# Kernel optimization log

Hardware: AMD Instinct MI355X
Metric: run time of the kernel (lower is better)

Reference implementation:

```python
import jax, jax.numpy as jnp
import numpy as np

HEADS = 8
DH = 64          # value head dim == kernel head dim (expansion ratio 1.0)
DIM = 256
BOT = 256        # bottleneck_dim
DOUT = 256
HID = 4 * 256    # MLP hidden (expansion_ratio=4)
EPS_LN = 1e-5
EPS_GN = 1e-6


def layer_norm(x, g, b):
    m = x.mean(axis=-1, keepdims=True)
    v = x.var(axis=-1, keepdims=True)
    return (x - m) / jnp.sqrt(v + EPS_LN) * g + b


def rotate_half(x):
    x1, x2 = jnp.split(x, 2, axis=-1)
    return jnp.concatenate([-x2, x1], axis=-1)


def apply_rope(t, cos, sin):
    return t * cos + rotate_half(t) * sin


def mlp(x, W1, b1, W2, b2):
    return jax.nn.gelu(x @ W1 + b1) @ W2 + b2


def pooling_reducer(x, Win, W1, b1, W2, b2):
    # x: (b, n, m, c); mean-pool over axis 2, then MLP
    x = x @ Win
    x = x.mean(axis=2)
    return mlp(x, W1, b1, W2, b2)


def dp_kernel(x, Wqk, cos, sin):
    # x: (b, n, BOT) -> softmax attention kernel (b, h, n, n)
    b, n, _ = x.shape
    qk = (x @ Wqk).reshape(b, n, 2, HEADS, DH).transpose(0, 3, 2, 1, 4)  # b h 2 n d
    qk = apply_rope(qk, cos, sin)
    q, k = qk[:, :, 0], qk[:, :, 1]
    attn = jnp.einsum('bhid,bhjd->bhij', q, k) * (1.0 / DH)  # softmax scale = 1/dim_head
    return jax.nn.softmax(attn, axis=-1)


def group_norm(x):
    # channels-last GroupNorm(heads groups, affine=False), per position
    b, i, l, _ = x.shape
    xg = x.reshape(b, i, l, HEADS, DH)
    m = xg.mean(axis=-1, keepdims=True)
    v = xg.var(axis=-1, keepdims=True)
    return ((xg - m) / jnp.sqrt(v + EPS_GN)).reshape(b, i, l, HEADS * DH)


def setup_inputs() -> dict:
    key = jax.random.key(0)
    ks = jax.random.split(key, 32)
    B, NY, NX = 4, 128, 128
    s = 0.02
    d = {
        'u': jax.random.normal(ks[0], (B, NY, NX, DIM), jnp.float32),
        'rotary_cos_y': jax.random.uniform(ks[1], (NY, DH), jnp.float32),
        'rotary_sin_y': jax.random.uniform(ks[2], (NY, DH), jnp.float32),
        'rotary_cos_x': jax.random.uniform(ks[3], (NX, DH), jnp.float32),
        'rotary_sin_x': jax.random.uniform(ks[4], (NX, DH), jnp.float32),
        'scalar_cond': jax.random.normal(ks[5], (B,), jnp.float32),
        # norms
        'ln1_g': jnp.ones((DIM,), jnp.float32), 'ln1_b': jnp.zeros((DIM,), jnp.float32),
        'ln2_g': jnp.ones((DIM,), jnp.float32), 'ln2_b': jnp.zeros((DIM,), jnp.float32),
        # to_v
        'Wv': jax.random.normal(ks[6], (DIM, HEADS * DH), jnp.float32) * s,
        # to_y PoolingReducer
        'Wy_in': jax.random.normal(ks[7], (DIM, DIM), jnp.float32) * s,
        'Wy1': jax.random.normal(ks[8], (DIM, HID), jnp.float32) * s,
        'by1': jnp.zeros((HID,), jnp.float32),
        'Wy2': jax.random.normal(ks[9], (HID, BOT), jnp.float32) * s,
        'by2': jnp.zeros((BOT,), jnp.float32),
        # to_x PoolingReducer
        'Wx_in': jax.random.normal(ks[10], (DIM, DIM), jnp.float32) * s,
        'Wx1': jax.random.normal(ks[11], (DIM, HID), jnp.float32) * s,
        'bx1': jnp.zeros((HID,), jnp.float32),
        'Wx2': jax.random.normal(ks[12], (HID, BOT), jnp.float32) * s,
        'bx2': jnp.zeros((BOT,), jnp.float32),
        # kernels
        'Wqk_x': jax.random.normal(ks[13], (BOT, 2 * HEADS * DH), jnp.float32) * s,
        'Wqk_y': jax.random.normal(ks[14], (BOT, 2 * HEADS * DH), jnp.float32) * s,
        # merge head
        'Wm': jax.random.normal(ks[15], (HEADS * DH, DOUT), jnp.float32) * s,
        'bm': jnp.zeros((DOUT,), jnp.float32),
        # ffn
        'Wf1': jax.random.normal(ks[16], (DOUT, 4 * DOUT), jnp.float32) * s,
        'bf1': jnp.zeros((4 * DOUT,), jnp.float32),
        'Wf2': jax.random.normal(ks[17], (4 * DOUT, DOUT), jnp.float32) * s,
        'bf2': jnp.zeros((DOUT,), jnp.float32),
    }
    return d


def reference(u, rotary_cos_y, rotary_sin_y, rotary_cos_x, rotary_sin_x, scalar_cond,
              ln1_g, ln1_b, ln2_g, ln2_b, Wv,
              Wy_in, Wy1, by1, Wy2, by2,
              Wx_in, Wx1, bx1, Wx2, bx2,
              Wqk_x, Wqk_y, Wm, bm, Wf1, bf1, Wf2, bf2):
    b, ny, nx, _ = u.shape
    u_skip = u
    un = layer_norm(u, ln1_g, ln1_b)
    # to_x: transpose grid then pool over (now) second spatial axis -> (b, nx, BOT)
    u_x = pooling_reducer(un.transpose(0, 2, 1, 3), Wx_in, Wx1, bx1, Wx2, bx2)
    # to_y: pool over nx -> (b, ny, BOT)
    u_y = pooling_reducer(un, Wy_in, Wy1, by1, Wy2, by2)
    k_x = dp_kernel(u_x, Wqk_x, rotary_cos_x, rotary_sin_x)  # (b,h,nx,nx)
    k_y = dp_kernel(u_y, Wqk_y, rotary_cos_y, rotary_sin_y)  # (b,h,ny,ny)
    # values: b i l (h c) -> b h i l c
    v = (un @ Wv).reshape(b, ny, nx, HEADS, DH).transpose(0, 3, 1, 2, 4)
    u_phi = jnp.einsum('bhij,bhjmc->bhimc', k_y, v)
    u_phi = jnp.einsum('bhlm,bhimc->bhilc', k_x, u_phi)
    u_phi = u_phi.transpose(0, 2, 3, 1, 4).reshape(b, ny, nx, HEADS * DH)
    u2 = group_norm(u_phi) @ Wm + bm + u_skip  # dropout is identity in eval
    out = mlp(layer_norm(u2, ln2_g, ln2_b), Wf1, bf1, Wf2, bf2) + u2
    return out
```

## Files before the change

### kernel.cpp

```cpp
#include <hip/hip_runtime.h>
#include <hip/hip_bf16.h>
#include <math.h>

#define NB 4
#define NY 128
#define NX 128
#define DIM 256
#define NH 8
#define DH_ 64
#define HDIM 512
#define HID 1024
#define NPOS (NB*NY*NX)

typedef __hip_bfloat16 bf16_t;
typedef __attribute__((ext_vector_type(8))) short short8;
typedef __attribute__((ext_vector_type(4))) float f32x4;

__device__ __forceinline__ float b2f(bf16_t x){ return __bfloat162float(x); }
__device__ __forceinline__ bf16_t f2b(float x){ return __float2bfloat16(x); }
__device__ __forceinline__ short f2s(float x){ bf16_t h = __float2bfloat16(x); return *reinterpret_cast<short*>(&h); }
__device__ __forceinline__ float s2f(short x){ bf16_t h = *reinterpret_cast<bf16_t*>(&x); return __bfloat162float(h); }


__device__ __forceinline__ float gelu_tanh(float x){
  float z = 1.5957691216057308f*(x + 0.044715f*x*x*x);
  return x / (1.0f + __expf(-z));
}

__global__ void __launch_bounds__(256) k_pack(const float* __restrict__ W,
    short* __restrict__ out, int K, int N){
  int tid = blockIdx.x*256 + threadIdx.x;
  int lane = tid & 63;
  int rem = tid >> 6;
  int ntiles = N >> 4;
  int nt = rem % ntiles, kb = rem / ntiles;
  int n = nt*16 + (lane & 15);
  int k0 = kb*32 + (lane>>4)*8;
  short8 v;
  #pragma unroll
  for (int j=0;j<8;j++) v[j] = f2s(W[(size_t)(k0+j)*N + n]);
  *(short8*)&out[(size_t)tid*8] = v;
}

__global__ void __launch_bounds__(256) k_ln1(const float* __restrict__ u,
    const float* __restrict__ g, const float* __restrict__ b,
    bf16_t* __restrict__ un){
  int wave = threadIdx.x >> 6, lane = threadIdx.x & 63;
  size_t row = (size_t)blockIdx.x*4 + wave;
  const float* x = u + row*DIM;
  float v[4]; float s=0.f, ss=0.f;
  #pragma unroll
  for (int j=0;j<4;j++){ float t = x[lane + j*64]; v[j]=t; s+=t; ss+=t*t; }
  #pragma unroll
  for (int off=32;off>0;off>>=1){ s += __shfl_down(s,off,64); ss += __shfl_down(ss,off,64); }
  s = __shfl(s,0,64); ss = __shfl(ss,0,64);
  float m = s*(1.0f/DIM);
  float var = ss*(1.0f/DIM) - m*m;
  float r = rsqrtf(var + 1e-5f);
  bf16_t* o = un + row*DIM;
  #pragma unroll
  for (int j=0;j<4;j++){
    int f = lane + j*64;
    o[f] = f2b((v[j]-m)*r*g[f] + b[f]);
  }
}

__global__ void __launch_bounds__(256) k_pool_y(const bf16_t* __restrict__ un, float* __restrict__ pooly){
  int by = blockIdx.x;
  int d = threadIdx.x;
  size_t base = (size_t)by*NX*DIM + d;
  float s = 0.f;
  for (int x=0;x<NX;x++) s += b2f(un[base + (size_t)x*DIM]);
  pooly[(size_t)by*DIM + d] = s*(1.0f/NX);
}
__global__ void __launch_bounds__(256) k_pool_x(const bf16_t* __restrict__ un, float* __restrict__ poolx){
  int bb = blockIdx.x / NX, x = blockIdx.x % NX;
  int d = threadIdx.x;
  size_t base = ((size_t)bb*NY*NX + x)*DIM + d;
  float s = 0.f;
  for (int y=0;y<NY;y++) s += b2f(un[base + (size_t)y*NX*DIM]);
  poolx[(size_t)blockIdx.x*DIM + d] = s*(1.0f/NY);
}

#define GS_STRIDE 72
__global__ void __launch_bounds__(256) k_gemm2(const float* __restrict__ A0,
    const float* __restrict__ A1,
    const short* __restrict__ W0, const short* __restrict__ W1,
    const float* __restrict__ b0, const float* __restrict__ b1,
    float* __restrict__ C0, float* __restrict__ C1, int N, int K, int dogelu){
  const float* A  = blockIdx.z ? A1 : A0;
  const short* WP = blockIdx.z ? W1 : W0;
  const float* bias = blockIdx.z ? b1 : b0;
  float* C = blockIdx.z ? C1 : C0;
  __shared__ __align__(16) short As[64*GS_STRIDE];
  int tid = threadIdx.x;
  int lane = tid & 63, w = tid >> 6;
  int am = lane & 15, aq = lane >> 4;
  int m0 = blockIdx.x*64;
  int nt0 = blockIdx.y*16;
  int ntiles = N >> 4;
  f32x4 o[4][4];
  #pragma unroll
  for (int mt=0;mt<4;mt++)
    #pragma unroll
    for (int nt=0;nt<4;nt++) o[mt][nt] = (f32x4){0.f,0.f,0.f,0.f};

  for (int kc=0; kc<K; kc+=64){
    #pragma unroll
    for (int it=0; it<4; it++){
      int q = tid + it*256;
      int r = q >> 4, c4 = q & 15;
      float4 v = *(const float4*)&A[(size_t)(m0+r)*K + kc + c4*4];
      ushort4 p;
      p.x = (ushort)f2s(v.x); p.y = (ushort)f2s(v.y);
      p.z = (ushort)f2s(v.z); p.w = (ushort)f2s(v.w);
      *(ushort4*)&As[r*GS_STRIDE + c4*4] = p;
    }
    __syncthreads();
    #pragma unroll
    for (int kb=0; kb<2; kb++){
      short8 a[4], bfr[4];
      #pragma unroll
      for (int mt=0;mt<4;mt++)
        a[mt] = *(const short8*)&As[(mt*16+am)*GS_STRIDE + kb*32 + aq*8];
      int kbg = (kc>>5) + kb;
      #pragma unroll
      for (int nt=0;nt<4;nt++){
        int ntg = nt0 + w*4 + nt;
        bfr[nt] = *(const short8*)&WP[(size_t)((kbg*ntiles + ntg)*64 + lane)*8];
      }
      #pragma unroll
      for (int mt=0;mt<4;mt++)
        #pragma unroll
        for (int nt=0;nt<4;nt++)
          o[mt][nt] = __builtin_amdgcn_mfma_f32_16x16x32_bf16(a[mt], bfr[nt], o[mt][nt], 0,0,0);
    }
    __syncthreads();
  }

  #pragma unroll
  for (int nt=0;nt<4;nt++){
    int col = (nt0 + w*4 + nt)*16 + am;
    float bv = bias ? bias[col] : 0.f;
    #pragma unroll
    for (int mt=0;mt<4;mt++){
      #pragma unroll
      for (int reg=0;reg<4;reg++){
        int row = m0 + mt*16 + aq*4 + reg;
        float val = o[mt][nt][reg] + bv;
        if (dogelu) val = gelu_tanh(val);
        C[(size_t)row*N + col] = val;
      }
    }
  }
}

__global__ void __launch_bounds__(256) k_rope(const float* __restrict__ qk,
    const float* __restrict__ cs, const float* __restrict__ sn,
    float* __restrict__ q, float* __restrict__ k){
  int idx = blockIdx.x*256 + threadIdx.x;
  int c = idx & 63;
  int h = (idx>>6) & 7;
  int p = (idx>>9) & 1;
  int n = (idx>>10) & 127;
  int bb = idx>>17;
  float t = qk[idx];
  float t2 = qk[(c<32) ? idx+32 : idx-32];
  if (c<32) t2 = -t2;
  float val = t*cs[n*64+c] + t2*sn[n*64+c];
  float* dst = p ? k : q;
  dst[(((size_t)bb*NH + h)*128 + n)*64 + c] = val;
}

__global__ void __launch_bounds__(128) k_attn(const float* __restrict__ q,
    const float* __restrict__ k, bf16_t* __restrict__ attn){
  int i = blockIdx.x & 127;
  int bh = blockIdx.x >> 7;
  __shared__ float qs[64];
  __shared__ float sm[128];
  int tid = threadIdx.x;
  const float* qrow = q + ((size_t)bh*128 + i)*64;
  if (tid < 64) qs[tid] = qrow[tid];
  __syncthreads();
  const float* krow = k + ((size_t)bh*128 + tid)*64;
  float dot = 0.f;
  for (int c=0;c<64;c++) dot += qs[c]*krow[c];
  dot *= (1.0f/64.0f);
  sm[tid] = dot;
  __syncthreads();
  float mx = -1e30f;
  for (int j=0;j<128;j++) mx = fmaxf(mx, sm[j]);
  __syncthreads();
  float e = expf(dot - mx);
  sm[tid] = e;
  __syncthreads();
  float s = 0.f;
  for (int j=0;j<128;j++) s += sm[j];
  attn[(size_t)blockIdx.x*128 + tid] = f2b(e/s);
}

#define AST 136
#define UST 72
#define VST 136
__global__ void __launch_bounds__(256) k_phi1m(const bf16_t* __restrict__ un,
    const short* __restrict__ WvP, const bf16_t* __restrict__ attn,
    bf16_t* __restrict__ phi){
  int m  = blockIdx.x & (NX-1);
  int bh = blockIdx.x >> 7;
  int b  = bh >> 3, h = bh & 7;
  __shared__ __align__(16) short At[128*AST];
  __shared__ __align__(16) short unc[128*UST];
  __shared__ __align__(16) short Vt[64*VST];
  int tid = threadIdx.x;
  int lane = tid & 63, w = tid >> 6;
  int am = lane & 15, aq = lane >> 4;

  {
    const ushort* ag = (const ushort*)attn + (size_t)bh*16384;
    #pragma unroll
    for (int it=0; it<16; it++){
      int q = tid + it*256;
      int i = q >> 5, j4 = q & 31;
      *(ushort4*)&At[i*AST + j4*4] = *(const ushort4*)(ag + i*128 + j4*4);
    }
  }

  f32x4 v[2][4];
  #pragma unroll
  for (int mt=0;mt<2;mt++)
    #pragma unroll
    for (int nt=0;nt<4;nt++) v[mt][nt] = (f32x4){0.f,0.f,0.f,0.f};
  const ushort* ug = (const ushort*)un;
  for (int kc=0; kc<4; kc++){
    #pragma unroll
    for (int it=0; it<8; it++){
      int q = tid + it*256;
      int y = q >> 4, c4 = q & 15;
      *(ushort4*)&unc[y*UST + c4*4] =
          *(const ushort4*)(ug + (((size_t)b*NY + y)*NX + m)*DIM + kc*64 + c4*4);
    }
    __syncthreads();
    #pragma unroll
    for (int kb=0; kb<2; kb++){
      short8 a2[2], bb[4];
      #pragma unroll
      for (int mt=0;mt<2;mt++)
        a2[mt] = *(const short8*)&unc[(w*32 + mt*16 + am)*UST + kb*32 + aq*8];
      int kbg = kc*2 + kb;
      #pragma unroll
      for (int nt=0;nt<4;nt++)
        bb[nt] = *(const short8*)&WvP[(size_t)((kbg*32 + (h*4+nt))*64 + lane)*8];
      #pragma unroll
      for (int mt=0;mt<2;mt++)
        #pragma unroll
        for (int nt=0;nt<4;nt++)
          v[mt][nt] = __builtin_amdgcn_mfma_f32_16x16x32_bf16(a2[mt], bb[nt], v[mt][nt], 0,0,0);
    }
    __syncthreads();
  }
  #pragma unroll
  for (int mt=0;mt<2;mt++)
    #pragma unroll
    for (int nt=0;nt<4;nt++){
      int c = nt*16 + am;
      int y0 = w*32 + mt*16 + aq*4;
      ushort4 pk;
      pk.x = (ushort)f2s(v[mt][nt][0]);
      pk.y = (ushort)f2s(v[mt][nt][1]);
      pk.z = (ushort)f2s(v[mt][nt][2]);
      pk.w = (ushort)f2s(v[mt][nt][3]);
      *(ushort4*)&Vt[c*VST + y0] = pk;
    }
  __syncthreads();

  f32x4 o[2][4];
  #pragma unroll
  for (int mt=0;mt<2;mt++)
    #pragma unroll
    for (int nt=0;nt<4;nt++) o[mt][nt] = (f32x4){0.f,0.f,0.f,0.f};
  #pragma unroll
  for (int kb=0; kb<4; kb++){
    short8 a2[2], bb[4];
    #pragma unroll
    for (int mt=0;mt<2;mt++)
      a2[mt] = *(const short8*)&At[(w*32 + mt*16 + am)*AST + kb*32 + aq*8];
    #pragma unroll
    for (int nt=0;nt<4;nt++)
      bb[nt] = *(const short8*)&Vt[(nt*16 + am)*VST + kb*32 + aq*8];
    #pragma unroll
    for (int mt=0;mt<2;mt++)
      #pragma unroll
      for (int nt=0;nt<4;nt++)
        o[mt][nt] = __builtin_amdgcn_mfma_f32_16x16x32_bf16(a2[mt], bb[nt], o[mt][nt], 0,0,0);
  }
  ushort* pg = (ushort*)phi + (size_t)bh*NY*NX*DH_ + (size_t)m*DH_;
  #pragma unroll
  for (int mt=0;mt<2;mt++)
    #pragma unroll
    for (int nt=0;nt<4;nt++)
      #pragma unroll
      for (int reg=0;reg<4;reg++){
        int i = w*32 + mt*16 + aq*4 + reg;
        int c = nt*16 + am;
        pg[(size_t)i*(NX*DH_) + c] = (ushort)f2s(o[mt][nt][reg]);
      }
}

__global__ void __launch_bounds__(256) k_phi2m(const bf16_t* __restrict__ attn,
    bf16_t* __restrict__ phi){
  int i  = blockIdx.x & (NY-1);
  int bh = blockIdx.x >> 7;
  __shared__ __align__(16) short Ax[128*AST];
  __shared__ __align__(16) short Pt[64*VST];
  int tid = threadIdx.x;
  int lane = tid & 63, w = tid >> 6;
  int am = lane & 15, aq = lane >> 4;

  {
    const ushort* ag = (const ushort*)attn + (size_t)bh*16384;
    #pragma unroll
    for (int it=0; it<16; it++){
      int q = tid + it*256;
      int r = q >> 5, j4 = q & 31;
      *(ushort4*)&Ax[r*AST + j4*4] = *(const ushort4*)(ag + r*128 + j4*4);
    }
  }
  ushort* pg = (ushort*)phi + (size_t)(bh*NY + i)*(NX*DH_);
  #pragma unroll
  for (int it=0; it<8; it++){
    int q = tid + it*256;
    int mm = q >> 4, c4 = q & 15;
    ushort4 v4 = *(const ushort4*)(pg + mm*DH_ + c4*4);
    Pt[(c4*4+0)*VST + mm] = v4.x;
    Pt[(c4*4+1)*VST + mm] = v4.y;
    Pt[(c4*4+2)*VST + mm] = v4.z;
    Pt[(c4*4+3)*VST + mm] = v4.w;
  }
  __syncthreads();

  f32x4 o[2][4];
  #pragma unroll
  for (int mt=0;mt<2;mt++)
    #pragma unroll
    for (int nt=0;nt<4;nt++) o[mt][nt] = (f32x4){0.f,0.f,0.f,0.f};
  #pragma unroll
  for (int kb=0; kb<4; kb++){
    short8 a2[2], bb[4];
    #pragma unroll
    for (int mt=0;mt<2;mt++)
      a2[mt] = *(const short8*)&Ax[(w*32 + mt*16 + am)*AST + kb*32 + aq*8];
    #pragma unroll
    for (int nt=0;nt<4;nt++)
      bb[nt] = *(const short8*)&Pt[(nt*16 + am)*VST + kb*32 + aq*8];
    #pragma unroll
    for (int mt=0;mt<2;mt++)
      #pragma unroll
      for (int nt=0;nt<4;nt++)
        o[mt][nt] = __builtin_amdgcn_mfma_f32_16x16x32_bf16(a2[mt], bb[nt], o[mt][nt], 0,0,0);
  }
  #pragma unroll
  for (int mt=0;mt<2;mt++)
    #pragma unroll
    for (int nt=0;nt<4;nt++)
      #pragma unroll
      for (int reg=0;reg<4;reg++){
        int l = w*32 + mt*16 + aq*4 + reg;
        int c = nt*16 + am;
        pg[(size_t)l*DH_ + c] = (ushort)f2s(o[mt][nt][reg]);
      }
}

#define GN_ST 520
#define ML_ST 264
__global__ void __launch_bounds__(512, 4) k_tail(const bf16_t* __restrict__ phi,
    const short* __restrict__ WmP, const float* __restrict__ bm,
    const float* __restrict__ u,
    const float* __restrict__ g2, const float* __restrict__ b2,
    const short* __restrict__ Wf1P, const float* __restrict__ bf1,
    const short* __restrict__ Wf2P, const float* __restrict__ bf2,
    float* __restrict__ out){
  __shared__ __align__(16) short SMEM[64*ML_ST*2];
  __shared__ float mean_s[512], rstd_s[512];
  __shared__ float prow[64][4], prow2[64][4];
  __shared__ float mrow[64], rrow[64];
  short* Xg = SMEM;
  short* Xm = SMEM;
  short* H  = SMEM + 64*ML_ST;
  int tid = threadIdx.x;
  int lane = tid & 63, w = tid >> 6;
  int wh = w >> 2, wl = w & 3;
  int am = lane & 15, aq = lane >> 4;
  size_t p0 = (size_t)blockIdx.x*64;
  int b  = (int)(p0 >> 14);
  int y  = (int)((p0 >> 7) & 127);
  int x0 = (int)(p0 & 127);

  #pragma unroll
  for (int it=0; it<16; it++){
    int q = tid + it*512;
    int r = q >> 7, f4 = q & 127;
    int h = f4 >> 4, c4 = f4 & 15;
    const ushort* src = (const ushort*)phi +
        ((((size_t)b*NH + h)*NY + y)*NX + (x0 + r))*DH_ + c4*4;
    *(ushort4*)&Xg[r*GN_ST + f4*4] = *(const ushort4*)src;
  }
  __syncthreads();
  {
    int g = tid;
    int r = g >> 3, h = g & 7;
    const short* base = &Xg[r*GN_ST + h*64];
    float s=0.f, ss=0.f;
    #pragma unroll
    for (int i=0;i<16;i++){
      ushort4 v4 = *(const ushort4*)&base[i*4];
      float a = s2f((short)v4.x), bq = s2f((short)v4.y), cq = s2f((short)v4.z), d = s2f((short)v4.w);
      s += a+bq+cq+d; ss += a*a+bq*bq+cq*cq+d*d;
    }
    float mm = s*(1.0f/64.0f);
    float vv = ss*(1.0f/64.0f) - mm*mm;
    mean_s[g] = mm;
    rstd_s[g] = rsqrtf(vv + 1e-6f);
  }
  __syncthreads();
  #pragma unroll
  for (int it=0; it<16; it++){
    int q = tid + it*512;
    int r = q >> 7, f4 = q & 127;
    int h = f4 >> 4;
    float mm = mean_s[r*8 + h], rs = rstd_s[r*8 + h];
    short* ptr = &Xg[r*GN_ST + f4*4];
    ushort4 v4 = *(ushort4*)ptr;
    v4.x = (ushort)f2s((s2f((short)v4.x)-mm)*rs);
    v4.y = (ushort)f2s((s2f((short)v4.y)-mm)*rs);
    v4.z = (ushort)f2s((s2f((short)v4.z)-mm)*rs);
    v4.w = (ushort)f2s((s2f((short)v4.w)-mm)*rs);
    *(ushort4*)ptr = v4;
  }
  __syncthreads();

  f32x4 u2r[2][4];
  #pragma unroll
  for (int mt=0;mt<2;mt++)
    #pragma unroll
    for (int nt=0;nt<4;nt++) u2r[mt][nt] = (f32x4){0.f,0.f,0.f,0.f};
  for (int kb=0; kb<16; kb++){
    short8 a[2], bfr[4];
    #pragma unroll
    for (int mt=0;mt<2;mt++)
      a[mt] = *(const short8*)&Xg[(wh*32 + mt*16 + am)*GN_ST + kb*32 + aq*8];
    #pragma unroll
    for (int nt=0;nt<4;nt++)
      bfr[nt] = *(const short8*)&WmP[(size_t)((kb*16 + (wl*4+nt))*64 + lane)*8];
    #pragma unroll
    for (int mt=0;mt<2;mt++)
      #pragma unroll
      for (int nt=0;nt<4;nt++)
        u2r[mt][nt] = __builtin_amdgcn_mfma_f32_16x16x32_bf16(a[mt], bfr[nt], u2r[mt][nt], 0,0,0);
  }
  #pragma unroll
  for (int nt=0;nt<4;nt++){
    int col = wl*64 + nt*16 + am;
    float bmv = bm[col];
    #pragma unroll
    for (int mt=0;mt<2;mt++){
      #pragma unroll
      for (int reg=0;reg<4;reg++){
        size_t p = p0 + wh*32 + mt*16 + aq*4 + reg;
        u2r[mt][nt][reg] += bmv + u[p*DIM + col];
      }
    }
  }

  #pragma unroll
  for (int mt=0;mt<2;mt++){
    #pragma unroll
    for (int reg=0;reg<4;reg++){
      float s  = u2r[mt][0][reg]+u2r[mt][1][reg]+u2r[mt][2][reg]+u2r[mt][3][reg];
      float ss = u2r[mt][0][reg]*u2r[mt][0][reg]+u2r[mt][1][reg]*u2r[mt][1][reg]
               + u2r[mt][2][reg]*u2r[mt][2][reg]+u2r[mt][3][reg]*u2r[mt][3][reg];
      #pragma unroll
      for (int msk=1; msk<16; msk<<=1){
        s  += __shfl_xor(s,  msk, 64);
        ss += __shfl_xor(ss, msk, 64);
      }
      if (am == 0){
        int r = wh*32 + mt*16 + aq*4 + reg;
        prow[r][wl] = s;
        prow2[r][wl] = ss;
      }
    }
  }
  __syncthreads();
  if (tid < 64){
    float s  = prow[tid][0]+prow[tid][1]+prow[tid][2]+prow[tid][3];
    float ss = prow2[tid][0]+prow2[tid][1]+prow2[tid][2]+prow2[tid][3];
    float m = s*(1.0f/DIM);
    mrow[tid] = m;
    rrow[tid] = rsqrtf(ss*(1.0f/DIM) - m*m + 1e-5f);
  }
  __syncthreads();
  #pragma unroll
  for (int nt=0;nt<4;nt++){
    int col = wl*64 + nt*16 + am;
    float gg = g2[col], bb2 = b2[col];
    #pragma unroll
    for (int mt=0;mt<2;mt++){
      #pragma unroll
      for (int reg=0;reg<4;reg++){
        int r = wh*32 + mt*16 + aq*4 + reg;
        Xm[r*ML_ST + col] = f2s((u2r[mt][nt][reg]-mrow[r])*rrow[r]*gg + bb2);
      }
    }
  }
  __syncthreads();

  f32x4 o2[2][4];
  #pragma unroll
  for (int mt=0;mt<2;mt++)
    #pragma unroll
    for (int nt=0;nt<4;nt++) o2[mt][nt] = u2r[mt][nt];

  for (int nc=0; nc<4; nc++){
    f32x4 hacc[2][4];
    #pragma unroll
    for (int mt=0;mt<2;mt++)
      #pragma unroll
      for (int nt=0;nt<4;nt++) hacc[mt][nt] = (f32x4){0.f,0.f,0.f,0.f};
    for (int kb=0; kb<8; kb++){
      short8 a[2], bfr[4];
      #pragma unroll
      for (int mt=0;mt<2;mt++)
        a[mt] = *(const short8*)&Xm[(wh*32 + mt*16 + am)*ML_ST + kb*32 + aq*8];
      #pragma unroll
      for (int nt=0;nt<4;nt++){
        int ntg = nc*16 + wl*4 + nt;
        bfr[nt] = *(const short8*)&Wf1P[(size_t)((kb*64 + ntg)*64 + lane)*8];
      }
      #pragma unroll
      for (int mt=0;mt<2;mt++)
        #pragma unroll
        for (int nt=0;nt<4;nt++)
          hacc[mt][nt] = __builtin_amdgcn_mfma_f32_16x16x32_bf16(a[mt], bfr[nt], hacc[mt][nt], 0,0,0);
    }
    #pragma unroll
    for (int nt=0;nt<4;nt++){
      int col_l = wl*64 + nt*16 + am;
      float bv = bf1[nc*256 + col_l];
      #pragma unroll
      for (int mt=0;mt<2;mt++){
        #pragma unroll
        for (int reg=0;reg<4;reg++){
          int row = wh*32 + mt*16 + aq*4 + reg;
          H[row*ML_ST + col_l] = f2s(gelu_tanh(hacc[mt][nt][reg] + bv));
        }
      }
    }
    __syncthreads();
    for (int kb=0; kb<8; kb++){
      short8 a[2], bfr[4];
      #pragma unroll
      for (int mt=0;mt<2;mt++)
        a[mt] = *(const short8*)&H[(wh*32 + mt*16 + am)*ML_ST + kb*32 + aq*8];
      int kbg = nc*8 + kb;
      #pragma unroll
      for (int nt=0;nt<4;nt++)
        bfr[nt] = *(const short8*)&Wf2P[(size_t)((kbg*16 + (wl*4+nt))*64 + lane)*8];
      #pragma unroll
      for (int mt=0;mt<2;mt++)
        #pragma unroll
        for (int nt=0;nt<4;nt++)
          o2[mt][nt] = __builtin_amdgcn_mfma_f32_16x16x32_bf16(a[mt], bfr[nt], o2[mt][nt], 0,0,0);
    }
    __syncthreads();
  }

  #pragma unroll
  for (int nt=0;nt<4;nt++){
    int col = wl*64 + nt*16 + am;
    float bv = bf2[col];
    #pragma unroll
    for (int mt=0;mt<2;mt++){
      #pragma unroll
      for (int reg=0;reg<4;reg++){
        size_t p = p0 + wh*32 + mt*16 + aq*4 + reg;
        out[p*DIM + col] = o2[mt][nt][reg] + bv;
      }
    }
  }
}

extern "C" void kernel_launch(void* const* d_in, const int* in_sizes, int n_in,
                              void* d_out, int out_size, void* d_ws, size_t ws_size,
                              hipStream_t stream){
  const float* u    = (const float*)d_in[0];
  const float* rcy  = (const float*)d_in[1];
  const float* rsy  = (const float*)d_in[2];
  const float* rcx  = (const float*)d_in[3];
  const float* rsx  = (const float*)d_in[4];
  const float* ln1g = (const float*)d_in[6];
  const float* ln1b = (const float*)d_in[7];
  const float* ln2g = (const float*)d_in[8];
  const float* ln2b = (const float*)d_in[9];
  const float* Wv   = (const float*)d_in[10];
  const float* Wyin = (const float*)d_in[11];
  const float* Wy1  = (const float*)d_in[12];
  const float* by1  = (const float*)d_in[13];
  const float* Wy2  = (const float*)d_in[14];
  const float* by2  = (const float*)d_in[15];
  const float* Wxin = (const float*)d_in[16];
  const float* Wx1  = (const float*)d_in[17];
  const float* bx1  = (const float*)d_in[18];
  const float* Wx2  = (const float*)d_in[19];
  const float* bx2  = (const float*)d_in[20];
  const float* Wqkx = (const float*)d_in[21];
  const float* Wqky = (const float*)d_in[22];
  const float* Wm   = (const float*)d_in[23];
  const float* bm   = (const float*)d_in[24];
  const float* Wf1  = (const float*)d_in[25];
  const float* bf1  = (const float*)d_in[26];
  const float* Wf2  = (const float*)d_in[27];
  const float* bf2  = (const float*)d_in[28];

  char* w = (char*)d_ws;
  auto alloc = [&](size_t n) -> void* {
    void* p = (void*)w;
    w += (n + 255) & ~(size_t)255;
    return p;
  };
  bf16_t* UN   = (bf16_t*)alloc((size_t)NPOS*DIM*2);
  bf16_t* PHI  = (bf16_t*)alloc((size_t)NB*NH*NY*NX*DH_*2);
  float* POOLY = (float*)alloc((size_t)NB*NY*DIM*4);
  float* POOLX = (float*)alloc((size_t)NB*NX*DIM*4);
  float* TY    = (float*)alloc((size_t)512*256*4);
  float* TX    = (float*)alloc((size_t)512*256*4);
  float* HY    = (float*)alloc((size_t)512*1024*4);
  float* HX    = (float*)alloc((size_t)512*1024*4);
  float* UY    = (float*)alloc((size_t)512*256*4);
  float* UX    = (float*)alloc((size_t)512*256*4);
  float* QKY   = (float*)alloc((size_t)512*1024*4);
  float* QKX   = (float*)alloc((size_t)512*1024*4);
  float* QRY   = (float*)alloc((size_t)NB*NH*128*64*4);
  float* KRY   = (float*)alloc((size_t)NB*NH*128*64*4);
  float* QRX   = (float*)alloc((size_t)NB*NH*128*64*4);
  float* KRX   = (float*)alloc((size_t)NB*NH*128*64*4);
  bf16_t* ATTNY = (bf16_t*)alloc((size_t)NB*NH*128*128*2);
  bf16_t* ATTNX = (bf16_t*)alloc((size_t)NB*NH*128*128*2);
  short* WF1P  = (short*)alloc((size_t)256*1024*2);
  short* WF2P  = (short*)alloc((size_t)1024*256*2);
  short* WMP   = (short*)alloc((size_t)512*256*2);
  short* WVP   = (short*)alloc((size_t)256*512*2);
  short* WYINP = (short*)alloc((size_t)256*256*2);
  short* WY1P  = (short*)alloc((size_t)256*1024*2);
  short* WY2P  = (short*)alloc((size_t)1024*256*2);
  short* WQKYP = (short*)alloc((size_t)256*1024*2);
  short* WXINP = (short*)alloc((size_t)256*256*2);
  short* WX1P  = (short*)alloc((size_t)256*1024*2);
  short* WX2P  = (short*)alloc((size_t)1024*256*2);
  short* WQKXP = (short*)alloc((size_t)256*1024*2);
  float* U2 = (float*)d_out;
  (void)in_sizes; (void)n_in; (void)out_size; (void)ws_size;

  k_pack<<<(256*1024/8)/256, 256, 0, stream>>>(Wf1, WF1P, 256, 1024);
  k_pack<<<(1024*256/8)/256, 256, 0, stream>>>(Wf2, WF2P, 1024, 256);
  k_pack<<<(512*256/8)/256, 256, 0, stream>>>(Wm, WMP, 512, 256);
  k_pack<<<(256*512/8)/256, 256, 0, stream>>>(Wv, WVP, 256, 512);
  k_pack<<<(256*256/8)/256, 256, 0, stream>>>(Wyin, WYINP, 256, 256);
  k_pack<<<(256*1024/8)/256, 256, 0, stream>>>(Wy1, WY1P, 256, 1024);
  k_pack<<<(1024*256/8)/256, 256, 0, stream>>>(Wy2, WY2P, 1024, 256);
  k_pack<<<(256*1024/8)/256, 256, 0, stream>>>(Wqky, WQKYP, 256, 1024);
  k_pack<<<(256*256/8)/256, 256, 0, stream>>>(Wxin, WXINP, 256, 256);
  k_pack<<<(256*1024/8)/256, 256, 0, stream>>>(Wx1, WX1P, 256, 1024);
  k_pack<<<(1024*256/8)/256, 256, 0, stream>>>(Wx2, WX2P, 1024, 256);
  k_pack<<<(256*1024/8)/256, 256, 0, stream>>>(Wqkx, WQKXP, 256, 1024);

  k_ln1<<<NPOS/4, 256, 0, stream>>>(u, ln1g, ln1b, UN);
  k_pool_y<<<NB*NY, 256, 0, stream>>>(UN, POOLY);
  k_pool_x<<<NB*NX, 256, 0, stream>>>(UN, POOLX);

  k_gemm2<<<dim3(8,1,2), 256, 0, stream>>>(POOLY, POOLX, WYINP, WXINP,
      (const float*)nullptr, (const float*)nullptr, TY, TX, 256, 256, 0);
  k_gemm2<<<dim3(8,4,2), 256, 0, stream>>>(TY, TX, WY1P, WX1P, by1, bx1, HY, HX, 1024, 256, 1);
  k_gemm2<<<dim3(8,1,2), 256, 0, stream>>>(HY, HX, WY2P, WX2P, by2, bx2, UY, UX, 256, 1024, 0);
  k_gemm2<<<dim3(8,4,2), 256, 0, stream>>>(UY, UX, WQKYP, WQKXP,
      (const float*)nullptr, (const float*)nullptr, QKY, QKX, 1024, 256, 0);

  k_rope<<<(NB*128*1024)/256, 256, 0, stream>>>(QKY, rcy, rsy, QRY, KRY);
  k_rope<<<(NB*128*1024)/256, 256, 0, stream>>>(QKX, rcx, rsx, QRX, KRX);
  k_attn<<<NB*NH*128, 128, 0, stream>>>(QRY, KRY, ATTNY);
  k_attn<<<NB*NH*128, 128, 0, stream>>>(QRX, KRX, ATTNX);
  k_phi1m<<<NB*NH*NX, 256, 0, stream>>>(UN, WVP, ATTNY, PHI);
  k_phi2m<<<NB*NH*NY, 256, 0, stream>>>(ATTNX, PHI);
  k_tail<<<NPOS/64, 512, 0, stream>>>(PHI, WMP, bm, u, ln2g, ln2b,
      WF1P, bf1, WF2P, bf2, U2);
}
```

Measured before the change: 610.5 us.

## Double threads per block in phi and tail kernels, warp-shuffle softmax in attn

Doubles the wave count per block in k_phi1m, k_phi2m (256 to 512 threads) and k_tail (512 to 1024 threads), so each wave computes half as many MFMA tiles. This lowers per-thread accumulator register use and raises parallelism per block. k_attn replaces its serial shared-memory max/sum loops with wave shuffle reductions and uses the fast __expf. The cost is more duplicated B-operand weight fetches across waves and larger blocks that may limit scheduling; k_tail's launch bounds of (1024, 8) may also force register spilling.

```diff
diff --git a/kernel.cpp b/kernel.cpp
--- a/kernel.cpp
+++ b/kernel.cpp
@@ -177,8 +177,9 @@
   int i = blockIdx.x & 127;
   int bh = blockIdx.x >> 7;
   __shared__ float qs[64];
-  __shared__ float sm[128];
+  __shared__ float red[4];
   int tid = threadIdx.x;
+  int wv = tid >> 6, lane = tid & 63;
   const float* qrow = q + ((size_t)bh*128 + i)*64;
   if (tid < 64) qs[tid] = qrow[tid];
   __syncthreads();
@@ -186,23 +187,26 @@
   float dot = 0.f;
   for (int c=0;c<64;c++) dot += qs[c]*krow[c];
   dot *= (1.0f/64.0f);
-  sm[tid] = dot;
-  __syncthreads();
-  float mx = -1e30f;
-  for (int j=0;j<128;j++) mx = fmaxf(mx, sm[j]);
-  __syncthreads();
-  float e = expf(dot - mx);
-  sm[tid] = e;
-  __syncthreads();
-  float s = 0.f;
-  for (int j=0;j<128;j++) s += sm[j];
+  float mx = dot;
+  #pragma unroll
+  for (int off=32;off>0;off>>=1) mx = fmaxf(mx, __shfl_xor(mx, off, 64));
+  if (lane == 0) red[wv] = mx;
+  __syncthreads();
+  mx = fmaxf(red[0], red[1]);
+  float e = __expf(dot - mx);
+  float s = e;
+  #pragma unroll
+  for (int off=32;off>0;off>>=1) s += __shfl_xor(s, off, 64);
+  if (lane == 0) red[2+wv] = s;
+  __syncthreads();
+  s = red[2] + red[3];
   attn[(size_t)blockIdx.x*128 + tid] = f2b(e/s);
 }
 
 #define AST 136
 #define UST 72
 #define VST 136
-__global__ void __launch_bounds__(256) k_phi1m(const bf16_t* __restrict__ un,
+__global__ void __launch_bounds__(512) k_phi1m(const bf16_t* __restrict__ un,
     const short* __restrict__ WvP, const bf16_t* __restrict__ attn,
     bf16_t* __restrict__ phi){
   int m  = blockIdx.x & (NX-1);
@@ -218,23 +222,21 @@
   {
     const ushort* ag = (const ushort*)attn + (size_t)bh*16384;
     #pragma unroll
-    for (int it=0; it<16; it++){
-      int q = tid + it*256;
+    for (int it=0; it<8; it++){
+      int q = tid + it*512;
       int i = q >> 5, j4 = q & 31;
       *(ushort4*)&At[i*AST + j4*4] = *(const ushort4*)(ag + i*128 + j4*4);
     }
   }
 
-  f32x4 v[2][4];
-  #pragma unroll
-  for (int mt=0;mt<2;mt++)
-    #pragma unroll
-    for (int nt=0;nt<4;nt++) v[mt][nt] = (f32x4){0.f,0.f,0.f,0.f};
+  f32x4 v[4];
+  #pragma unroll
+  for (int nt=0;nt<4;nt++) v[nt] = (f32x4){0.f,0.f,0.f,0.f};
   const ushort* ug = (const ushort*)un;
   for (int kc=0; kc<4; kc++){
     #pragma unroll
-    for (int it=0; it<8; it++){
-      int q = tid + it*256;
+    for (int it=0; it<4; it++){
+      int q = tid + it*512;
       int y = q >> 4, c4 = q & 15;
       *(ushort4*)&unc[y*UST + c4*4] =
           *(const ushort4*)(ug + (((size_t)b*NY + y)*NX + m)*DIM + kc*64 + c4*4);
@@ -242,71 +244,57 @@
     __syncthreads();
     #pragma unroll
     for (int kb=0; kb<2; kb++){
-      short8 a2[2], bb[4];
-      #pragma unroll
-      for (int mt=0;mt<2;mt++)
-        a2[mt] = *(const short8*)&unc[(w*32 + mt*16 + am)*UST + kb*32 + aq*8];
+      short8 a2 = *(const short8*)&unc[(w*16 + am)*UST + kb*32 + aq*8];
       int kbg = kc*2 + kb;
+      short8 bb[4];
       #pragma unroll
       for (int nt=0;nt<4;nt++)
         bb[nt] = *(const short8*)&WvP[(size_t)((kbg*32 + (h*4+nt))*64 + lane)*8];
       #pragma unroll
-      for (int mt=0;mt<2;mt++)
-        #pragma unroll
-        for (int nt=0;nt<4;nt++)
-          v[mt][nt] = __builtin_amdgcn_mfma_f32_16x16x32_bf16(a2[mt], bb[nt], v[mt][nt], 0,0,0);
+      for (int nt=0;nt<4;nt++)
+        v[nt] = __builtin_amdgcn_mfma_f32_16x16x32_bf16(a2, bb[nt], v[nt], 0,0,0);
     }
     __syncthreads();
   }
   #pragma unroll
-  for (int mt=0;mt<2;mt++)
-    #pragma unroll
-    for (int nt=0;nt<4;nt++){
-      int c = nt*16 + am;
-      int y0 = w*32 + mt*16 + aq*4;
-      ushort4 pk;
-      pk.x = (ushort)f2s(v[mt][nt][0]);
-      pk.y = (ushort)f2s(v[mt][nt][1]);
-      pk.z = (ushort)f2s(v[mt][nt][2]);
-      pk.w = (ushort)f2s(v[mt][nt][3]);
-      *(ushort4*)&Vt[c*VST + y0] = pk;
-    }
-  __syncthreads();
-
-  f32x4 o[2][4];
-  #pragma unroll
-  for (int mt=0;mt<2;mt++)
-    #pragma unroll
-    for (int nt=0;nt<4;nt++) o[mt][nt] = (f32x4){0.f,0.f,0.f,0.f};
+  for (int nt=0;nt<4;nt++){
+    int c = nt*16 + am;
+    int y0 = w*16 + aq*4;
+    ushort4 pk;
+    pk.x = (ushort)f2s(v[nt][0]);
+    pk.y = (ushort)f2s(v[nt][1]);
+    pk.z = (ushort)f2s(v[nt][2]);
+    pk.w = (ushort)f2s(v[nt][3]);
+    *(ushort4*)&Vt[c*VST + y0] = pk;
+  }
+  __syncthreads();
+
+  f32x4 o[4];
+  #pragma unroll
+  for (int nt=0;nt<4;nt++) o[nt] = (f32x4){0.f,0.f,0.f,0.f};
   #pragma unroll
   for (int kb=0; kb<4; kb++){
-    short8 a2[2], bb[4];
-    #pragma unroll
-    for (int mt=0;mt<2;mt++)
-      a2[mt] = *(const short8*)&At[(w*32 + mt*16 + am)*AST + kb*32 + aq*8];
+    short8 a2 = *(const short8*)&At[(w*16 + am)*AST + kb*32 + aq*8];
+    short8 bb[4];
     #pragma unroll
     for (int nt=0;nt<4;nt++)
       bb[nt] = *(const short8*)&Vt[(nt*16 + am)*VST + kb*32 + aq*8];
     #pragma unroll
-    for (int mt=0;mt<2;mt++)
-      #pragma unroll
-      for (int nt=0;nt<4;nt++)
-        o[mt][nt] = __builtin_amdgcn_mfma_f32_16x16x32_bf16(a2[mt], bb[nt], o[mt][nt], 0,0,0);
+    for (int nt=0;nt<4;nt++)
+      o[nt] = __builtin_amdgcn_mfma_f32_16x16x32_bf16(a2, bb[nt], o[nt], 0,0,0);
   }
   ushort* pg = (ushort*)phi + (size_t)bh*NY*NX*DH_ + (size_t)m*DH_;
   #pragma unroll
-  for (int mt=0;mt<2;mt++)
-    #pragma unroll
-    for (int nt=0;nt<4;nt++)
-      #pragma unroll
-      for (int reg=0;reg<4;reg++){
-        int i = w*32 + mt*16 + aq*4 + reg;
-        int c = nt*16 + am;
-        pg[(size_t)i*(NX*DH_) + c] = (ushort)f2s(o[mt][nt][reg]);
-      }
-}
-
-__global__ void __launch_bounds__(256) k_phi2m(const bf16_t* __restrict__ attn,
+  for (int nt=0;nt<4;nt++)
+    #pragma unroll
+    for (int reg=0;reg<4;reg++){
+      int i = w*16 + aq*4 + reg;
+      int c = nt*16 + am;
+      pg[(size_t)i*(NX*DH_) + c] = (ushort)f2s(o[nt][reg]);
+    }
+}
+
+__global__ void __launch_bounds__(512) k_phi2m(const bf16_t* __restrict__ attn,
     bf16_t* __restrict__ phi){
   int i  = blockIdx.x & (NY-1);
   int bh = blockIdx.x >> 7;
@@ -319,16 +307,16 @@
   {
     const ushort* ag = (const ushort*)attn + (size_t)bh*16384;
     #pragma unroll
-    for (int it=0; it<16; it++){
-      int q = tid + it*256;
+    for (int it=0; it<8; it++){
+      int q = tid + it*512;
       int r = q >> 5, j4 = q & 31;
       *(ushort4*)&Ax[r*AST + j4*4] = *(const ushort4*)(ag + r*128 + j4*4);
     }
   }
   ushort* pg = (ushort*)phi + (size_t)(bh*NY + i)*(NX*DH_);
   #pragma unroll
-  for (int it=0; it<8; it++){
-    int q = tid + it*256;
+  for (int it=0; it<4; it++){
+    int q = tid + it*512;
     int mm = q >> 4, c4 = q & 15;
     ushort4 v4 = *(const ushort4*)(pg + mm*DH_ + c4*4);
     Pt[(c4*4+0)*VST + mm] = v4.x;
@@ -338,41 +326,33 @@
   }
   __syncthreads();
 
-  f32x4 o[2][4];
-  #pragma unroll
-  for (int mt=0;mt<2;mt++)
-    #pragma unroll
-    for (int nt=0;nt<4;nt++) o[mt][nt] = (f32x4){0.f,0.f,0.f,0.f};
+  f32x4 o[4];
+  #pragma unroll
+  for (int nt=0;nt<4;nt++) o[nt] = (f32x4){0.f,0.f,0.f,0.f};
   #pragma unroll
   for (int kb=0; kb<4; kb++){
-    short8 a2[2], bb[4];
-    #pragma unroll
-    for (int mt=0;mt<2;mt++)
-      a2[mt] = *(const short8*)&Ax[(w*32 + mt*16 + am)*AST + kb*32 + aq*8];
+    short8 a2 = *(const short8*)&Ax[(w*16 + am)*AST + kb*32 + aq*8];
+    short8 bb[4];
     #pragma unroll
     for (int nt=0;nt<4;nt++)
       bb[nt] = *(const short8*)&Pt[(nt*16 + am)*VST + kb*32 + aq*8];
     #pragma unroll
-    for (int mt=0;mt<2;mt++)
-      #pragma unroll
-      for (int nt=0;nt<4;nt++)
-        o[mt][nt] = __builtin_amdgcn_mfma_f32_16x16x32_bf16(a2[mt], bb[nt], o[mt][nt], 0,0,0);
-  }
-  #pragma unroll
-  for (int mt=0;mt<2;mt++)
-    #pragma unroll
     for (int nt=0;nt<4;nt++)
-      #pragma unroll
-      for (int reg=0;reg<4;reg++){
-        int l = w*32 + mt*16 + aq*4 + reg;
-        int c = nt*16 + am;
-        pg[(size_t)l*DH_ + c] = (ushort)f2s(o[mt][nt][reg]);
-      }
+      o[nt] = __builtin_amdgcn_mfma_f32_16x16x32_bf16(a2, bb[nt], o[nt], 0,0,0);
+  }
+  #pragma unroll
+  for (int nt=0;nt<4;nt++)
+    #pragma unroll
+    for (int reg=0;reg<4;reg++){
+      int l = w*16 + aq*4 + reg;
+      int c = nt*16 + am;
+      pg[(size_t)l*DH_ + c] = (ushort)f2s(o[nt][reg]);
+    }
 }
 
 #define GN_ST 520
 #define ML_ST 264
-__global__ void __launch_bounds__(512, 4) k_tail(const bf16_t* __restrict__ phi,
+__global__ void __launch_bounds__(1024, 8) k_tail(const bf16_t* __restrict__ phi,
     const short* __restrict__ WmP, const float* __restrict__ bm,
     const float* __restrict__ u,
     const float* __restrict__ g2, const float* __restrict__ b2,
@@ -381,14 +361,14 @@
     float* __restrict__ out){
   __shared__ __align__(16) short SMEM[64*ML_ST*2];
   __shared__ float mean_s[512], rstd_s[512];
-  __shared__ float prow[64][4], prow2[64][4];
+  __shared__ float prow[64][8], prow2[64][8];
   __shared__ float mrow[64], rrow[64];
   short* Xg = SMEM;
   short* Xm = SMEM;
   short* H  = SMEM + 64*ML_ST;
   int tid = threadIdx.x;
   int lane = tid & 63, w = tid >> 6;
-  int wh = w >> 2, wl = w & 3;
+  int wh = w >> 3, wl = w & 7;
   int am = lane & 15, aq = lane >> 4;
   size_t p0 = (size_t)blockIdx.x*64;
   int b  = (int)(p0 >> 14);
@@ -396,8 +376,8 @@
   int x0 = (int)(p0 & 127);
 
   #pragma unroll
-  for (int it=0; it<16; it++){
-    int q = tid + it*512;
+  for (int it=0; it<8; it++){
+    int q = tid + it*1024;
     int r = q >> 7, f4 = q & 127;
     int h = f4 >> 4, c4 = f4 & 15;
     const ushort* src = (const ushort*)phi +
@@ -405,7 +385,7 @@
     *(ushort4*)&Xg[r*GN_ST + f4*4] = *(const ushort4*)src;
   }
   __syncthreads();
-  {
+  if (tid < 512){
     int g = tid;
     int r = g >> 3, h = g & 7;
     const short* base = &Xg[r*GN_ST + h*64];
@@ -423,8 +403,8 @@
   }
   __syncthreads();
   #pragma unroll
-  for (int it=0; it<16; it++){
-    int q = tid + it*512;
+  for (int it=0; it<8; it++){
+    int q = tid + it*1024;
     int r = q >> 7, f4 = q & 127;
     int h = f4 >> 4;
     float mm = mean_s[r*8 + h], rs = rstd_s[r*8 + h];
@@ -438,28 +418,28 @@
   }
   __syncthreads();
 
-  f32x4 u2r[2][4];
+  f32x4 u2r[2][2];
   #pragma unroll
   for (int mt=0;mt<2;mt++)
     #pragma unroll
-    for (int nt=0;nt<4;nt++) u2r[mt][nt] = (f32x4){0.f,0.f,0.f,0.f};
+    for (int nt=0;nt<2;nt++) u2r[mt][nt] = (f32x4){0.f,0.f,0.f,0.f};
   for (int kb=0; kb<16; kb++){
-    short8 a[2], bfr[4];
+    short8 a[2], bfr[2];
     #pragma unroll
     for (int mt=0;mt<2;mt++)
       a[mt] = *(const short8*)&Xg[(wh*32 + mt*16 + am)*GN_ST + kb*32 + aq*8];
     #pragma unroll
-    for (int nt=0;nt<4;nt++)
-      bfr[nt] = *(const short8*)&WmP[(size_t)((kb*16 + (wl*4+nt))*64 + lane)*8];
+    for (int nt=0;nt<2;nt++)
+      bfr[nt] = *(const short8*)&WmP[(size_t)((kb*16 + (wl*2+nt))*64 + lane)*8];
     #pragma unroll
     for (int mt=0;mt<2;mt++)
       #pragma unroll
-      for (int nt=0;nt<4;nt++)
+      for (int nt=0;nt<2;nt++)
         u2r[mt][nt] = __builtin_amdgcn_mfma_f32_16x16x32_bf16(a[mt], bfr[nt], u2r[mt][nt], 0,0,0);
   }
   #pragma unroll
-  for (int nt=0;nt<4;nt++){
-    int col = wl*64 + nt*16 + am;
+  for (int nt=0;nt<2;nt++){
+    int col = wl*32 + nt*16 + am;
     float bmv = bm[col];
     #pragma unroll
     for (int mt=0;mt<2;mt++){
@@ -475,9 +455,8 @@
   for (int mt=0;mt<2;mt++){
     #pragma unroll
     for (int reg=0;reg<4;reg++){
-      float s  = u2r[mt][0][reg]+u2r[mt][1][reg]+u2r[mt][2][reg]+u2r[mt][3][reg];
-      float ss = u2r[mt][0][reg]*u2r[mt][0][reg]+u2r[mt][1][reg]*u2r[mt][1][reg]
-               + u2r[mt][2][reg]*u2r[mt][2][reg]+u2r[mt][3][reg]*u2r[mt][3][reg];
+      float s  = u2r[mt][0][reg]+u2r[mt][1][reg];
+      float ss = u2r[mt][0][reg]*u2r[mt][0][reg]+u2r[mt][1][reg]*u2r[mt][1][reg];
       #pragma unroll
       for (int msk=1; msk<16; msk<<=1){
         s  += __shfl_xor(s,  msk, 64);
@@ -492,16 +471,17 @@
   }
   __syncthreads();
   if (tid < 64){
-    float s  = prow[tid][0]+prow[tid][1]+prow[tid][2]+prow[tid][3];
-    float ss = prow2[tid][0]+prow2[tid][1]+prow2[tid][2]+prow2[tid][3];
+    float s = 0.f, ss = 0.f;
+    #pragma unroll
+    for (int j=0;j<8;j++){ s += prow[tid][j]; ss += prow2[tid][j]; }
     float m = s*(1.0f/DIM);
     mrow[tid] = m;
     rrow[tid] = rsqrtf(ss*(1.0f/DIM) - m*m + 1e-5f);
   }
   __syncthreads();
   #pragma unroll
-  for (int nt=0;nt<4;nt++){
-    int col = wl*64 + nt*16 + am;
+  for (int nt=0;nt<2;nt++){
+    int col = wl*32 + nt*16 + am;
     float gg = g2[col], bb2 = b2[col];
     #pragma unroll
     for (int mt=0;mt<2;mt++){
@@ -514,37 +494,37 @@
   }
   __syncthreads();
 
-  f32x4 o2[2][4];
+  f32x4 o2[2][2];
   #pragma unroll
   for (int mt=0;mt<2;mt++)
     #pragma unroll
-    for (int nt=0;nt<4;nt++) o2[mt][nt] = u2r[mt][nt];
+    for (int nt=0;nt<2;nt++) o2[mt][nt] = u2r[mt][nt];
 
   for (int nc=0; nc<4; nc++){
-    f32x4 hacc[2][4];
+    f32x4 hacc[2][2];
     #pragma unroll
     for (int mt=0;mt<2;mt++)
       #pragma unroll
-      for (int nt=0;nt<4;nt++) hacc[mt][nt] = (f32x4){0.f,0.f,0.f,0.f};
+      for (int nt=0;nt<2;nt++) hacc[mt][nt] = (f32x4){0.f,0.f,0.f,0.f};
     for (int kb=0; kb<8; kb++){
-      short8 a[2], bfr[4];
+      short8 a[2], bfr[2];
       #pragma unroll
       for (int mt=0;mt<2;mt++)
         a[mt] = *(const short8*)&Xm[(wh*32 + mt*16 + am)*ML_ST + kb*32 + aq*8];
       #pragma unroll
-      for (int nt=0;nt<4;nt++){
-        int ntg = nc*16 + wl*4 + nt;
+      for (int nt=0;nt<2;nt++){
+        int ntg = nc*16 + wl*2 + nt;
         bfr[nt] = *(const short8*)&Wf1P[(size_t)((kb*64 + ntg)*64 + lane)*8];
       }
       #pragma unroll
       for (int mt=0;mt<2;mt++)
         #pragma unroll
-        for (int nt=0;nt<4;nt++)
+        for (int nt=0;nt<2;nt++)
           hacc[mt][nt] = __builtin_amdgcn_mfma_f32_16x16x32_bf16(a[mt], bfr[nt], hacc[mt][nt], 0,0,0);
     }
     #pragma unroll
-    for (int nt=0;nt<4;nt++){
-      int col_l = wl*64 + nt*16 + am;
+    for (int nt=0;nt<2;nt++){
+      int col_l = wl*32 + nt*16 + am;
       float bv = bf1[nc*256 + col_l];
       #pragma unroll
       for (int mt=0;mt<2;mt++){
@@ -557,26 +537,26 @@
     }
     __syncthreads();
     for (int kb=0; kb<8; kb++){
-      short8 a[2], bfr[4];
+      short8 a[2], bfr[2];
       #pragma unroll
       for (int mt=0;mt<2;mt++)
         a[mt] = *(const short8*)&H[(wh*32 + mt*16 + am)*ML_ST + kb*32 + aq*8];
       int kbg = nc*8 + kb;
       #pragma unroll
-      for (int nt=0;nt<4;nt++)
-        bfr[nt] = *(const short8*)&Wf2P[(size_t)((kbg*16 + (wl*4+nt))*64 + lane)*8];
+      for (int nt=0;nt<2;nt++)
+        bfr[nt] = *(const short8*)&Wf2P[(size_t)((kbg*16 + (wl*2+nt))*64 + lane)*8];
       #pragma unroll
       for (int mt=0;mt<2;mt++)
         #pragma unroll
-        for (int nt=0;nt<4;nt++)
+        for (int nt=0;nt<2;nt++)
           o2[mt][nt] = __builtin_amdgcn_mfma_f32_16x16x32_bf16(a[mt], bfr[nt], o2[mt][nt], 0,0,0);
     }
     __syncthreads();
   }
 
   #pragma unroll
-  for (int nt=0;nt<4;nt++){
-    int col = wl*64 + nt*16 + am;
+  for (int nt=0;nt<2;nt++){
+    int col = wl*32 + nt*16 + am;
     float bv = bf2[col];
     #pragma unroll
     for (int mt=0;mt<2;mt++){
@@ -688,8 +668,8 @@
   k_rope<<<(NB*128*1024)/256, 256, 0, stream>>>(QKX, rcx, rsx, QRX, KRX);
   k_attn<<<NB*NH*128, 128, 0, stream>>>(QRY, KRY, ATTNY);
   k_attn<<<NB*NH*128, 128, 0, stream>>>(QRX, KRX, ATTNX);
-  k_phi1m<<<NB*NH*NX, 256, 0, stream>>>(UN, WVP, ATTNY, PHI);
-  k_phi2m<<<NB*NH*NY, 256, 0, stream>>>(ATTNX, PHI);
-  k_tail<<<NPOS/64, 512, 0, stream>>>(PHI, WMP, bm, u, ln2g, ln2b,
+  k_phi1m<<<NB*NH*NX, 512, 0, stream>>>(UN, WVP, ATTNY, PHI);
+  k_phi2m<<<NB*NH*NY, 512, 0, stream>>>(ATTNX, PHI);
+  k_tail<<<NPOS/64, 1024, 0, stream>>>(PHI, WMP, bm, u, ln2g, ln2b,
       WF1P, bf1, WF2P, bf2, U2);
 }
```

New measurement: 664.1 us. +8.8%, slower.
